# Performance work log

Hardware: AMD Instinct MI355X
Metric: run time of the kernel (lower is better)

The kernel has to match this reference:

```python
import jax, jax.numpy as jnp
import numpy as np

D_MODEL = 768
NUM_HEADS = 12
HEAD_DIM = D_MODEL // NUM_HEADS
D_FF = 3072
LN_EPS = 1e-5


def _xavier(key, shape):
    # nn.init.xavier_uniform_ on a [out, in] Linear weight
    fan_out, fan_in = shape[-2], shape[-1]
    limit = float(np.sqrt(6.0 / (fan_in + fan_out)))
    return jax.random.uniform(key, shape, jnp.float32, -limit, limit)


def setup_inputs() -> dict:
    key = jax.random.key(0)
    ks = jax.random.split(key, 10)
    x = jax.random.normal(ks[0], (4, 2048, D_MODEL), jnp.float32)
    # per-head projections stacked: [H, head_dim, d_model] (torch Linear weight layout [out, in])
    Wq = _xavier(ks[1], (NUM_HEADS, HEAD_DIM, D_MODEL))
    Wk = _xavier(ks[2], (NUM_HEADS, HEAD_DIM, D_MODEL))
    Wv = _xavier(ks[3], (NUM_HEADS, HEAD_DIM, D_MODEL))
    Wo = _xavier(ks[4], (D_MODEL, D_MODEL))
    W1 = jax.random.normal(ks[5], (D_FF, D_MODEL), jnp.float32) * 0.02
    b1 = jnp.zeros((D_FF,), jnp.float32)
    W2 = jax.random.normal(ks[6], (D_MODEL, D_FF), jnp.float32) * 0.02
    b2 = jnp.zeros((D_MODEL,), jnp.float32)
    g1 = jnp.ones((D_MODEL,), jnp.float32)
    be1 = jnp.zeros((D_MODEL,), jnp.float32)
    g2 = jnp.ones((D_MODEL,), jnp.float32)
    be2 = jnp.zeros((D_MODEL,), jnp.float32)
    return {"x": x, "Wq": Wq, "Wk": Wk, "Wv": Wv, "Wo": Wo,
            "W1": W1, "b1": b1, "W2": W2, "b2": b2,
            "g1": g1, "be1": be1, "g2": g2, "be2": be2}


def _layernorm(x, g, b):
    mu = jnp.mean(x, axis=-1, keepdims=True)
    var = jnp.mean(jnp.square(x - mu), axis=-1, keepdims=True)
    return (x - mu) * jax.lax.rsqrt(var + LN_EPS) * g + b


def reference(x, Wq, Wk, Wv, Wo, W1, b1, W2, b2, g1, be1, g2, be2):
    B, S, D = x.shape
    # all heads batched (same math as the per-head Python loop + concat)
    q = jnp.einsum('bsd,hed->bhse', x, Wq)   # [B,H,S,e]
    k = jnp.einsum('bsd,hed->bhse', x, Wk)
    v = jnp.einsum('bsd,hed->bhse', x, Wv)
    scores = jnp.einsum('bhse,bhte->bhst', q, k) / jnp.sqrt(jnp.float32(HEAD_DIM))
    attn = jax.nn.softmax(scores, axis=-1)
    ctx = jnp.einsum('bhst,bhte->bhse', attn, v)
    # concat heads along feature dim (head order matches stacking order)
    concat = ctx.transpose(0, 2, 1, 3).reshape(B, S, D)
    attn_out = concat @ Wo.T
    h = _layernorm(x + attn_out, g1, be1)
    ffn = jax.nn.relu(h @ W1.T + b1) @ W2.T + b2
    out = _layernorm(h + ffn, g2, be2)
    return out
```

## Files before the change

kernel.cpp:

```cpp
#include <hip/hip_runtime.h>

typedef unsigned short u16;
typedef unsigned int u32;
typedef __attribute__((ext_vector_type(8))) short short8;
typedef __attribute__((ext_vector_type(4))) float f32x4;
typedef __attribute__((ext_vector_type(4))) unsigned short u16x4;

__device__ __forceinline__ float b2f(u16 u){
  union { float f; unsigned int i; } c; c.i = ((unsigned int)u) << 16; return c.f;
}
__device__ __forceinline__ u16 f2b(float f){
  union { float f; unsigned int i; } c; c.f = f;
  unsigned int i = c.i;
  unsigned int r = (i + 0x7FFFu + ((i >> 16) & 1u)) >> 16;
  return (u16)r;
}

#define EXP2(x) exp2f(x)

#define GLD16(gp, lp) __builtin_amdgcn_global_load_lds( \
    (const __attribute__((address_space(1))) void*)(gp), \
    (__attribute__((address_space(3))) void*)(lp), 16, 0, 0)

__device__ __forceinline__ u32 pkbf(float lo, float hi){
  u32 r;
  asm volatile("v_cvt_pk_bf16_f32 %0, %1, %2" : "=v"(r) : "v"(lo), "v"(hi));
  return r;
}

__global__ __launch_bounds__(256) void cvt_all(
    const float* __restrict__ s0, const float* __restrict__ s1,
    const float* __restrict__ s2, const float* __restrict__ s3,
    const float* __restrict__ s4, const float* __restrict__ s5,
    const float* __restrict__ s6, u16* __restrict__ dst)
{
  const int i = (blockIdx.x * 256 + threadIdx.x) * 4;
  const float* sp;
  if      (i <  6291456) sp = s0 + i;
  else if (i <  6881280) sp = s1 + (i - 6291456);
  else if (i <  7471104) sp = s2 + (i - 6881280);
  else if (i <  8060928) sp = s3 + (i - 7471104);
  else if (i <  8650752) sp = s4 + (i - 8060928);
  else if (i < 11010048) sp = s5 + (i - 8650752);
  else                   sp = s6 + (i - 11010048);
  float4 f = *(const float4*)sp;
  u16x4 o = { f2b(f.x), f2b(f.y), f2b(f.z), f2b(f.w) };
  *(u16x4*)(dst + i) = o;
}

__global__ __launch_bounds__(256) void transpose_v(const u16* __restrict__ v,
                                                   u16* __restrict__ vt){
  __shared__ short t[64][72];
  const int plane = blockIdx.y;
  const u16* vp = v + (size_t)plane * 2048 * 64;
  u16* vtp = vt + (size_t)plane * 2048 * 64;
  const int s0 = blockIdx.x * 64;
#pragma unroll
  for (int j = 0; j < 2; j++){
    int ch = threadIdx.x + 256*j;
    int r = ch >> 3, c = (ch & 7) << 3;
    short8 val = *(const short8*)(vp + (size_t)(s0 + r)*64 + c);
#pragma unroll
    for (int jj = 0; jj < 8; jj++) t[c + jj][r] = val[jj];
  }
  __syncthreads();
#pragma unroll
  for (int j = 0; j < 2; j++){
    int ch = threadIdx.x + 256*j;
    int r = ch >> 3, c = (ch & 7) << 3;
    *(short8*)(vtp + (size_t)r*2048 + s0 + c) = *(const short8*)&t[r][c];
  }
}

enum { EPI_QKV = 0, EPI_WO = 1, EPI_FFN1 = 2, EPI_FFN2 = 3 };
__device__ __forceinline__ float KSCALE_C(){ return 0.125f * 1.44269504088896340736f; }

template<int EPI>
__global__ __launch_bounds__(256) void gemm_bt(
    const u16* __restrict__ A, const u16* __restrict__ Bm,
    int K, int gx,
    u16* __restrict__ outB,
    const float* __restrict__ auxF,
    const u16* __restrict__ auxB)
{
  __shared__ __align__(16) short Asm[128][32];
  __shared__ __align__(16) short Bsm[128][32];
  const int tid  = threadIdx.x;
  const int lane = tid & 63;
  const int wid  = tid >> 6;
  const int wr = wid >> 1, wc = wid & 1;
  const int fr = lane & 15, fq = lane >> 4;

  const int nwg = gridDim.x;
  const int lin = blockIdx.x;
  const int wg  = (lin & 7) * (nwg >> 3) + (lin >> 3);
  const int bx = wg % gx, by = wg / gx;
  const int m0 = by * 128, n0 = bx * 128;

  f32x4 acc[4][4];
#pragma unroll
  for (int i = 0; i < 4; i++)
#pragma unroll
    for (int j = 0; j < 4; j++) acc[i][j] = (f32x4){0.f, 0.f, 0.f, 0.f};

  const int lrow = lane >> 2;
  const int lcol = (lane & 3) << 3;

  for (int k0 = 0; k0 < K; k0 += 32) {
    const u16* ga = A  + (size_t)(m0 + wid*32 + lrow) * K + k0 + lcol;
    const u16* gb = Bm + (size_t)(n0 + wid*32 + lrow) * K + k0 + lcol;
    GLD16(ga,                 &Asm[wid*32][0]);
    GLD16(ga + (size_t)16*K,  &Asm[wid*32 + 16][0]);
    GLD16(gb,                 &Bsm[wid*32][0]);
    GLD16(gb + (size_t)16*K,  &Bsm[wid*32 + 16][0]);
    __syncthreads();

    short8 a[4], b[4];
#pragma unroll
    for (int i = 0; i < 4; i++) a[i] = *(const short8*)&Asm[wr*64 + i*16 + fr][fq*8];
#pragma unroll
    for (int j = 0; j < 4; j++) b[j] = *(const short8*)&Bsm[wc*64 + j*16 + fr][fq*8];
    __builtin_amdgcn_s_setprio(1);
#pragma unroll
    for (int i = 0; i < 4; i++)
#pragma unroll
      for (int j = 0; j < 4; j++)
        acc[i][j] = __builtin_amdgcn_mfma_f32_16x16x32_bf16(a[i], b[j], acc[i][j], 0, 0, 0);
    __builtin_amdgcn_s_setprio(0);
    __syncthreads();
  }

#pragma unroll
  for (int i = 0; i < 4; i++) {
    const int row0 = m0 + wr*64 + i*16 + fq*4;
#pragma unroll
    for (int j = 0; j < 4; j++) {
      const int col = n0 + wc*64 + j*16 + fr;
#pragma unroll
      for (int r = 0; r < 4; r++) {
        const int row = row0 + r;
        float val = acc[i][j][r];
        if (EPI == EPI_QKV) {
          int tt = (col >= 1536) ? 2 : (col >= 768 ? 1 : 0);
          int rem = col - tt * 768;
          int h = rem >> 6, e = rem & 63;
          int bb = row >> 11, s = row & 2047;
          size_t idx = (((size_t)(tt*48 + bb*12 + h)) * 2048 + s) * 64 + e;
          if (tt == 1) val *= KSCALE_C();
          outB[idx] = f2b(val);
        } else if (EPI == EPI_WO) {
          size_t idx = (size_t)row * 768 + col;
          outB[idx] = f2b(val + b2f(auxB[idx]));
        } else if (EPI == EPI_FFN1) {
          float o = val + auxF[col];
          o = o > 0.f ? o : 0.f;
          outB[(size_t)row * 3072 + col] = f2b(o);
        } else {
          size_t idx = (size_t)row * 768 + col;
          outB[idx] = f2b(val + auxF[col] + b2f(auxB[idx]));
        }
      }
    }
  }
}

__global__ __launch_bounds__(256) void flash_attn(
    const u16* __restrict__ q, const u16* __restrict__ kmat, const u16* __restrict__ vtmat,
    u16* __restrict__ ctx)
{
  const int tid = threadIdx.x;
  const int lane = tid & 63, wid = tid >> 6;
  const int fr = lane & 15, fq = lane >> 4;
  const int orig = blockIdx.x;
  const int wg = (orig & 7) * 192 + (orig >> 3);
  const int qb = wg & 31;
  const int ph = wg >> 5;
  const size_t plane = (size_t)ph * 2048 * 64;
  const u16* qp  = q + plane;
  const u16* kp  = kmat + plane;
  const u16* vtp = vtmat + plane;

  __shared__ __align__(16) short Ksm[2][64][64];
  __shared__ __align__(16) short Vsm[2][64][64];

  const int qr0 = qb*64 + wid*16;
  const short8 aq0 = *(const short8*)(qp + (size_t)(qr0 + fr)*64 + fq*8);
  const short8 aq1 = *(const short8*)(qp + (size_t)(qr0 + fr)*64 + 32 + fq*8);

  short8 vones;
#pragma unroll
  for (int j = 0; j < 8; j++) vones[j] = (short)0x3F80;

  const int rA = wid*16 + (lane >> 3);
  const int rB = rA + 8;
  const int cA = (((lane & 7) ^ ((rA & 3) | (((rA >> 3) & 1) << 2)))) * 8;
  const int cB = (((lane & 7) ^ ((rB & 3) | (((rB >> 3) & 1) << 2)))) * 8;

#define STAGE(B, KT) do { \
    GLD16(kp  + (size_t)((KT)*64 + rA)*64 + cA,  &Ksm[B][wid*16    ][0]); \
    GLD16(kp  + (size_t)((KT)*64 + rB)*64 + cB,  &Ksm[B][wid*16 + 8][0]); \
    GLD16(vtp + (size_t)rA*2048 + (KT)*64 + cA,  &Vsm[B][wid*16    ][0]); \
    GLD16(vtp + (size_t)rB*2048 + (KT)*64 + cB,  &Vsm[B][wid*16 + 8][0]); \
  } while(0)

  f32x4 o[4];
#pragma unroll
  for (int eb = 0; eb < 4; eb++) o[eb] = (f32x4){0.f, 0.f, 0.f, 0.f};
  float m = -1e30f, l = 0.f;
  const f32x4 zero = (f32x4){0.f, 0.f, 0.f, 0.f};

  STAGE(0, 0);
  __syncthreads();

  const int fK  = (fr & 3) | (((fr >> 2) & 1) << 2);
  const int kc0 = ((fq    ) ^ fK) * 8;
  const int kc1 = ((4 + fq) ^ fK) * 8;
  const int krow = (fr & 3) + 8 * (fr >> 2);
  const int fV  = (fr & 3) | (((fr >> 3) & 1) << 2);
  const int vc0 = ((fq    ) ^ fV) * 8;
  const int vc1 = ((4 + fq) ^ fV) * 8;

  int buf = 0;
  for (int kt = 0; kt < 32; ++kt) {
    if (kt < 31) STAGE(buf ^ 1, kt + 1);

    f32x4 st[2][2];
    __builtin_amdgcn_s_setprio(1);
#pragma unroll
    for (int h = 0; h < 2; h++)
#pragma unroll
      for (int c = 0; c < 2; c++) {
        const short* kr = &Ksm[buf][32*h + 4*c + krow][0];
        short8 kf0 = *(const short8*)(kr + kc0);
        short8 kf1 = *(const short8*)(kr + kc1);
        f32x4 a = __builtin_amdgcn_mfma_f32_16x16x32_bf16(kf0, aq0, zero, 0, 0, 0);
        st[h][c]  = __builtin_amdgcn_mfma_f32_16x16x32_bf16(kf1, aq1, a,    0, 0, 0);
      }
    __builtin_amdgcn_s_setprio(0);

    float t0 = fmaxf(fmaxf(st[0][0][0], st[0][0][1]), st[0][0][2]);
    float t1 = fmaxf(fmaxf(st[0][0][3], st[0][1][0]), st[0][1][1]);
    float t2 = fmaxf(fmaxf(st[0][1][2], st[0][1][3]), st[1][0][0]);
    float t3 = fmaxf(fmaxf(st[1][0][1], st[1][0][2]), st[1][0][3]);
    float t4 = fmaxf(fmaxf(st[1][1][0], st[1][1][1]), st[1][1][2]);
    float u0 = fmaxf(fmaxf(t0, t1), st[1][1][3]);
    float u1 = fmaxf(fmaxf(t2, t3), t4);
    float lm = fmaxf(u0, u1);
    lm = fmaxf(lm, __shfl_xor(lm, 16));
    lm = fmaxf(lm, __shfl_xor(lm, 32));

    if (!__all(lm <= m + 8.f)) {
      float nm = fmaxf(m, lm);
      float corr = EXP2(m - nm);
      m = nm;
      l *= corr;
#pragma unroll
      for (int eb = 0; eb < 4; eb++)
#pragma unroll
        for (int r = 0; r < 4; r++) o[eb][r] *= corr;
    }

    float p[2][2][4];
#pragma unroll
    for (int h = 0; h < 2; h++)
#pragma unroll
      for (int c = 0; c < 2; c++)
#pragma unroll
        for (int r = 0; r < 4; r++)
          p[h][c][r] = EXP2(st[h][c][r] - m);

    union { u32 u[4]; short8 s8; } pf0, pf1;
    pf0.u[0] = pkbf(p[0][0][0], p[0][0][1]);
    pf0.u[1] = pkbf(p[0][0][2], p[0][0][3]);
    pf0.u[2] = pkbf(p[0][1][0], p[0][1][1]);
    pf0.u[3] = pkbf(p[0][1][2], p[0][1][3]);
    pf1.u[0] = pkbf(p[1][0][0], p[1][0][1]);
    pf1.u[1] = pkbf(p[1][0][2], p[1][0][3]);
    pf1.u[2] = pkbf(p[1][1][0], p[1][1][1]);
    pf1.u[3] = pkbf(p[1][1][2], p[1][1][3]);

    __builtin_amdgcn_s_setprio(1);
    f32x4 ol = __builtin_amdgcn_mfma_f32_16x16x32_bf16(vones, pf0.s8, zero, 0, 0, 0);
    ol       = __builtin_amdgcn_mfma_f32_16x16x32_bf16(vones, pf1.s8, ol,   0, 0, 0);
#pragma unroll
    for (int eb = 0; eb < 4; eb++) {
      const short* vr = &Vsm[buf][eb*16 + fr][0];
      o[eb] = __builtin_amdgcn_mfma_f32_16x16x32_bf16(*(const short8*)(vr + vc0), pf0.s8, o[eb], 0, 0, 0);
      o[eb] = __builtin_amdgcn_mfma_f32_16x16x32_bf16(*(const short8*)(vr + vc1), pf1.s8, o[eb], 0, 0, 0);
    }
    __builtin_amdgcn_s_setprio(0);
    l += ol[0];

    __syncthreads();
    buf ^= 1;
  }
#undef STAGE

  const float inv = 1.0f / l;
  const int s = qr0 + fr;
  u16* cp = ctx + ((size_t)((ph/12)*2048 + s)) * 768 + (ph%12)*64;
#pragma unroll
  for (int eb = 0; eb < 4; eb++) {
    u16x4 w = { f2b(o[eb][0]*inv), f2b(o[eb][1]*inv), f2b(o[eb][2]*inv), f2b(o[eb][3]*inv) };
    *(u16x4*)(cp + eb*16 + fq*4) = w;
  }
}

template<int F32OUT>
__global__ __launch_bounds__(256) void ln_k(const u16* __restrict__ in,
    const float* __restrict__ g, const float* __restrict__ be, void* __restrict__ outp)
{
  const int lane = threadIdx.x & 63, wid = threadIdx.x >> 6;
  const int row = blockIdx.x * 4 + wid;
  const u16* p = in + (size_t)row * 768;
  float v[12];
  float s = 0.f, s2 = 0.f;
#pragma unroll
  for (int i = 0; i < 6; i++) {
    ushort2 uv = *(const ushort2*)(p + i*128 + lane*2);
    v[2*i]   = b2f(uv.x);
    v[2*i+1] = b2f(uv.y);
    s += v[2*i] + v[2*i+1];
    s2 += v[2*i]*v[2*i] + v[2*i+1]*v[2*i+1];
  }
#pragma unroll
  for (int msk = 1; msk < 64; msk <<= 1) { s += __shfl_xor(s, msk); s2 += __shfl_xor(s2, msk); }
  const float mu = s * (1.f/768.f);
  const float var = s2 * (1.f/768.f) - mu*mu;
  const float rstd = rsqrtf(var + 1e-5f);
#pragma unroll
  for (int i = 0; i < 6; i++) {
    int c = i*128 + lane*2;
    float o0 = (v[2*i]   - mu) * rstd * g[c]   + be[c];
    float o1 = (v[2*i+1] - mu) * rstd * g[c+1] + be[c+1];
    if (F32OUT) {
      float2 w = { o0, o1 };
      *(float2*)((float*)outp + (size_t)row*768 + c) = w;
    } else {
      ushort2 w = { f2b(o0), f2b(o1) };
      *(ushort2*)((u16*)outp + (size_t)row*768 + c) = w;
    }
  }
}

extern "C" void kernel_launch(void* const* d_in, const int* in_sizes, int n_in,
                              void* d_out, int out_size, void* d_ws, size_t ws_size,
                              hipStream_t stream)
{
  const float* x   = (const float*)d_in[0];
  const float* Wq  = (const float*)d_in[1];
  const float* Wk  = (const float*)d_in[2];
  const float* Wv  = (const float*)d_in[3];
  const float* Wo  = (const float*)d_in[4];
  const float* W1  = (const float*)d_in[5];
  const float* b1  = (const float*)d_in[6];
  const float* W2  = (const float*)d_in[7];
  const float* b2  = (const float*)d_in[8];
  const float* g1  = (const float*)d_in[9];
  const float* be1 = (const float*)d_in[10];
  const float* g2  = (const float*)d_in[11];
  const float* be2 = (const float*)d_in[12];
  float* out = (float*)d_out;

  char* ws = (char*)d_ws;
  u16* xb     = (u16*)(ws + 0);
  u16* Wqkv_b = (u16*)(ws + 12582912);
  u16* Wo_b   = (u16*)(ws + 16121856);
  u16* W1_b   = (u16*)(ws + 17301504);
  u16* W2_b   = (u16*)(ws + 22020096);
  u16* qkv    = (u16*)(ws + 26738688);
  u16* ctxb   = (u16*)(ws + 64487424);
  u16* hidden = (u16*)(ws + 26738688);
  u16* vt     = (u16*)(ws + 77070336);
  u16* resid1 = (u16*)(ws + 77070336);
  u16* hb     = (u16*)(ws + 102236160);
  u16* pre2   = (u16*)(ws + 77070336);

  cvt_all<<<dim3(13056), 256, 0, stream>>>(x, Wq, Wk, Wv, Wo, W1, W2, (u16*)ws);

  gemm_bt<EPI_QKV><<<dim3(1152), 256, 0, stream>>>(
      xb, Wqkv_b, 768, 18, qkv, nullptr, nullptr);

  u16* qb_ = qkv;
  u16* kb_ = qkv + 6291456;
  u16* vb_ = qkv + 12582912;

  transpose_v<<<dim3(32, 48), 256, 0, stream>>>(vb_, vt);

  flash_attn<<<dim3(1536), 256, 0, stream>>>(qb_, kb_, vt, ctxb);

  gemm_bt<EPI_WO><<<dim3(384), 256, 0, stream>>>(
      ctxb, Wo_b, 768, 6, resid1, nullptr, xb);

  ln_k<0><<<2048, 256, 0, stream>>>(resid1, g1, be1, hb);

  gemm_bt<EPI_FFN1><<<dim3(1536), 256, 0, stream>>>(
      hb, W1_b, 768, 24, hidden, b1, nullptr);

  gemm_bt<EPI_FFN2><<<dim3(384), 256, 0, stream>>>(
      hidden, W2_b, 3072, 6, pre2, b2, hb);

  ln_k<1><<<2048, 256, 0, stream>>>(pre2, g2, be2, out);
}
```

Measured before the change: 328.3 us.

## Use 64x128 GEMM tiles for QKV/Wo/FFN2 and 128-row flash-attn blocks

Adds a gemm_bt64 kernel with 64x128 output tiles, used for the QKV, Wo and FFN2 projections. This doubles the grid size so the small-N GEMMs fill more compute units. The original 128x128 gemm_bt is kept only for FFN1. Flash attention moves to 512-thread blocks covering 128 query rows, so each staged K/V tile is shared by 8 waves, which halves the number of K/V tile loads. The cost is less reuse per GEMM tile and possibly lower occupancy for the larger attention blocks.

Result: no change. 323.2 us (-1.6%).

```diff
diff --git a/kernel.cpp b/kernel.cpp
--- a/kernel.cpp
+++ b/kernel.cpp
@@ -133,6 +133,80 @@
 #pragma unroll
   for (int i = 0; i < 4; i++) {
     const int row0 = m0 + wr*64 + i*16 + fq*4;
+#pragma unroll
+    for (int j = 0; j < 4; j++) {
+      const int col = n0 + wc*64 + j*16 + fr;
+#pragma unroll
+      for (int r = 0; r < 4; r++) {
+        const int row = row0 + r;
+        float val = acc[i][j][r];
+        if (EPI == EPI_FFN1) {
+          float o = val + auxF[col];
+          o = o > 0.f ? o : 0.f;
+          outB[(size_t)row * 3072 + col] = f2b(o);
+        }
+      }
+    }
+  }
+}
+
+template<int EPI>
+__global__ __launch_bounds__(256) void gemm_bt64(
+    const u16* __restrict__ A, const u16* __restrict__ Bm,
+    int K, int gx,
+    u16* __restrict__ outB,
+    const float* __restrict__ auxF,
+    const u16* __restrict__ auxB)
+{
+  __shared__ __align__(16) short Asm[64][32];
+  __shared__ __align__(16) short Bsm[128][32];
+  const int tid  = threadIdx.x;
+  const int lane = tid & 63;
+  const int wid  = tid >> 6;
+  const int wr = wid >> 1, wc = wid & 1;
+  const int fr = lane & 15, fq = lane >> 4;
+
+  const int nwg = gridDim.x;
+  const int lin = blockIdx.x;
+  const int wg  = (lin & 7) * (nwg >> 3) + (lin >> 3);
+  const int bx = wg % gx, by = wg / gx;
+  const int m0 = by * 64, n0 = bx * 128;
+
+  f32x4 acc[2][4];
+#pragma unroll
+  for (int i = 0; i < 2; i++)
+#pragma unroll
+    for (int j = 0; j < 4; j++) acc[i][j] = (f32x4){0.f, 0.f, 0.f, 0.f};
+
+  const int lrow = lane >> 2;
+  const int lcol = (lane & 3) << 3;
+
+  for (int k0 = 0; k0 < K; k0 += 32) {
+    const u16* ga = A  + (size_t)(m0 + wid*16 + lrow) * K + k0 + lcol;
+    const u16* gb = Bm + (size_t)(n0 + wid*32 + lrow) * K + k0 + lcol;
+    GLD16(ga,                 &Asm[wid*16][0]);
+    GLD16(gb,                 &Bsm[wid*32][0]);
+    GLD16(gb + (size_t)16*K,  &Bsm[wid*32 + 16][0]);
+    __syncthreads();
+
+    short8 a[2], b[4];
+#pragma unroll
+    for (int i = 0; i < 2; i++) a[i] = *(const short8*)&Asm[wr*32 + i*16 + fr][fq*8];
+#pragma unroll
+    for (int j = 0; j < 4; j++) b[j] = *(const short8*)&Bsm[wc*64 + j*16 + fr][fq*8];
+    __builtin_amdgcn_s_setprio(1);
+#pragma unroll
+    for (int i = 0; i < 2; i++)
+#pragma unroll
+      for (int j = 0; j < 4; j++)
+        acc[i][j] = __builtin_amdgcn_mfma_f32_16x16x32_bf16(a[i], b[j], acc[i][j], 0, 0, 0);
+    __builtin_amdgcn_s_setprio(0);
+    __syncthreads();
+  }
+
+#pragma unroll
+  for (int i = 0; i < 2; i++) {
+    const int row0 = m0 + wr*32 + i*16 + fq*4;
 #pragma unroll
     for (int j = 0; j < 4; j++) {
       const int col = n0 + wc*64 + j*16 + fr;
@@ -151,10 +225,6 @@
         } else if (EPI == EPI_WO) {
           size_t idx = (size_t)row * 768 + col;
           outB[idx] = f2b(val + b2f(auxB[idx]));
-        } else if (EPI == EPI_FFN1) {
-          float o = val + auxF[col];
-          o = o > 0.f ? o : 0.f;
-          outB[(size_t)row * 3072 + col] = f2b(o);
         } else {
           size_t idx = (size_t)row * 768 + col;
           outB[idx] = f2b(val + auxF[col] + b2f(auxB[idx]));
@@ -164,7 +234,7 @@
   }
 }
 
-__global__ __launch_bounds__(256) void flash_attn(
+__global__ __launch_bounds__(512) void flash_attn(
     const u16* __restrict__ q, const u16* __restrict__ kmat, const u16* __restrict__ vtmat,
     u16* __restrict__ ctx)
 {
@@ -172,9 +242,9 @@
   const int lane = tid & 63, wid = tid >> 6;
   const int fr = lane & 15, fq = lane >> 4;
   const int orig = blockIdx.x;
-  const int wg = (orig & 7) * 192 + (orig >> 3);
-  const int qb = wg & 31;
-  const int ph = wg >> 5;
+  const int wg = (orig & 7) * 96 + (orig >> 3);
+  const int qb = wg & 15;
+  const int ph = wg >> 4;
   const size_t plane = (size_t)ph * 2048 * 64;
   const u16* qp  = q + plane;
   const u16* kp  = kmat + plane;
@@ -183,7 +253,7 @@
   __shared__ __align__(16) short Ksm[2][64][64];
   __shared__ __align__(16) short Vsm[2][64][64];
 
-  const int qr0 = qb*64 + wid*16;
+  const int qr0 = qb*128 + wid*16;
   const short8 aq0 = *(const short8*)(qp + (size_t)(qr0 + fr)*64 + fq*8);
   const short8 aq1 = *(const short8*)(qp + (size_t)(qr0 + fr)*64 + 32 + fq*8);
 
@@ -191,16 +261,12 @@
 #pragma unroll
   for (int j = 0; j < 8; j++) vones[j] = (short)0x3F80;
 
-  const int rA = wid*16 + (lane >> 3);
-  const int rB = rA + 8;
+  const int rA = wid*8 + (lane >> 3);
   const int cA = (((lane & 7) ^ ((rA & 3) | (((rA >> 3) & 1) << 2)))) * 8;
-  const int cB = (((lane & 7) ^ ((rB & 3) | (((rB >> 3) & 1) << 2)))) * 8;
 
 #define STAGE(B, KT) do { \
-    GLD16(kp  + (size_t)((KT)*64 + rA)*64 + cA,  &Ksm[B][wid*16    ][0]); \
-    GLD16(kp  + (size_t)((KT)*64 + rB)*64 + cB,  &Ksm[B][wid*16 + 8][0]); \
-    GLD16(vtp + (size_t)rA*2048 + (KT)*64 + cA,  &Vsm[B][wid*16    ][0]); \
-    GLD16(vtp + (size_t)rB*2048 + (KT)*64 + cB,  &Vsm[B][wid*16 + 8][0]); \
+    GLD16(kp  + (size_t)((KT)*64 + rA)*64 + cA,  &Ksm[B][wid*8][0]); \
+    GLD16(vtp + (size_t)rA*2048 + (KT)*64 + cA,  &Vsm[B][wid*8][0]); \
   } while(0)
 
   f32x4 o[4];
@@ -378,7 +444,7 @@
 
   cvt_all<<<dim3(13056), 256, 0, stream>>>(x, Wq, Wk, Wv, Wo, W1, W2, (u16*)ws);
 
-  gemm_bt<EPI_QKV><<<dim3(1152), 256, 0, stream>>>(
+  gemm_bt64<EPI_QKV><<<dim3(2304), 256, 0, stream>>>(
       xb, Wqkv_b, 768, 18, qkv, nullptr, nullptr);
 
   u16* qb_ = qkv;
@@ -387,9 +453,9 @@
 
   transpose_v<<<dim3(32, 48), 256, 0, stream>>>(vb_, vt);
 
-  flash_attn<<<dim3(1536), 256, 0, stream>>>(qb_, kb_, vt, ctxb);
-
-  gemm_bt<EPI_WO><<<dim3(384), 256, 0, stream>>>(
+  flash_attn<<<dim3(768), 512, 0, stream>>>(qb_, kb_, vt, ctxb);
+
+  gemm_bt64<EPI_WO><<<dim3(768), 256, 0, stream>>>(
       ctxb, Wo_b, 768, 6, resid1, nullptr, xb);
 
   ln_k<0><<<2048, 256, 0, stream>>>(resid1, g1, be1, hb);
@@ -397,7 +463,7 @@
   gemm_bt<EPI_FFN1><<<dim3(1536), 256, 0, stream>>>(
       hb, W1_b, 768, 24, hidden, b1, nullptr);
 
-  gemm_bt<EPI_FFN2><<<dim3(384), 256, 0, stream>>>(
+  gemm_bt64<EPI_FFN2><<<dim3(768), 256, 0, stream>>>(
       hidden, W2_b, 3072, 6, pre2, b2, hb);
 
   ln_k<1><<<2048, 256, 0, stream>>>(pre2, g2, be2, out);
```

## Use 512-thread flash-attention blocks and fold running max into MFMA accumulator init

Applied to the files above, without the earlier changes.

Each attention workgroup now has 8 waves covering 128 query rows, so each staged 64-key K/V tile serves twice as many rows and each thread issues half as many global-to-LDS loads. The running maximum is kept as a negated offset and fed in as the initial accumulator of the QK^T MFMA, which removes the per-element subtraction before exp2 in the common no-rescale path. The trade-off is half as many blocks (768), with a larger block that may lower occupancy and scheduling flexibility. The epilogue outside the shown hunks must still match the new row mapping.

Measured after the change: 321.2 us. 1.02x faster.

```diff
diff --git a/kernel.cpp b/kernel.cpp
--- a/kernel.cpp
+++ b/kernel.cpp
@@ -164,7 +164,7 @@
   }
 }
 
-__global__ __launch_bounds__(256) void flash_attn(
+__global__ __launch_bounds__(512) void flash_attn(
     const u16* __restrict__ q, const u16* __restrict__ kmat, const u16* __restrict__ vtmat,
     u16* __restrict__ ctx)
 {
@@ -172,9 +172,9 @@
   const int lane = tid & 63, wid = tid >> 6;
   const int fr = lane & 15, fq = lane >> 4;
   const int orig = blockIdx.x;
-  const int wg = (orig & 7) * 192 + (orig >> 3);
-  const int qb = wg & 31;
-  const int ph = wg >> 5;
+  const int wg = (orig & 7) * 96 + (orig >> 3);
+  const int qb = wg & 15;
+  const int ph = wg >> 4;
   const size_t plane = (size_t)ph * 2048 * 64;
   const u16* qp  = q + plane;
   const u16* kp  = kmat + plane;
@@ -183,7 +183,7 @@
   __shared__ __align__(16) short Ksm[2][64][64];
   __shared__ __align__(16) short Vsm[2][64][64];
 
-  const int qr0 = qb*64 + wid*16;
+  const int qr0 = qb*128 + wid*16;
   const short8 aq0 = *(const short8*)(qp + (size_t)(qr0 + fr)*64 + fq*8);
   const short8 aq1 = *(const short8*)(qp + (size_t)(qr0 + fr)*64 + 32 + fq*8);
 
@@ -191,22 +191,18 @@
 #pragma unroll
   for (int j = 0; j < 8; j++) vones[j] = (short)0x3F80;
 
-  const int rA = wid*16 + (lane >> 3);
-  const int rB = rA + 8;
+  const int rA = wid*8 + (lane >> 3);
   const int cA = (((lane & 7) ^ ((rA & 3) | (((rA >> 3) & 1) << 2)))) * 8;
-  const int cB = (((lane & 7) ^ ((rB & 3) | (((rB >> 3) & 1) << 2)))) * 8;
 
 #define STAGE(B, KT) do { \
-    GLD16(kp  + (size_t)((KT)*64 + rA)*64 + cA,  &Ksm[B][wid*16    ][0]); \
-    GLD16(kp  + (size_t)((KT)*64 + rB)*64 + cB,  &Ksm[B][wid*16 + 8][0]); \
-    GLD16(vtp + (size_t)rA*2048 + (KT)*64 + cA,  &Vsm[B][wid*16    ][0]); \
-    GLD16(vtp + (size_t)rB*2048 + (KT)*64 + cB,  &Vsm[B][wid*16 + 8][0]); \
+    GLD16(kp  + (size_t)((KT)*64 + rA)*64 + cA,  &Ksm[B][wid*8][0]); \
+    GLD16(vtp + (size_t)rA*2048 + (KT)*64 + cA,  &Vsm[B][wid*8][0]); \
   } while(0)
 
   f32x4 o[4];
 #pragma unroll
   for (int eb = 0; eb < 4; eb++) o[eb] = (f32x4){0.f, 0.f, 0.f, 0.f};
-  float m = -1e30f, l = 0.f;
+  float mneg = 0.f, l = 0.f;
   const f32x4 zero = (f32x4){0.f, 0.f, 0.f, 0.f};
 
   STAGE(0, 0);
@@ -225,6 +221,7 @@
     if (kt < 31) STAGE(buf ^ 1, kt + 1);
 
     f32x4 st[2][2];
+    const f32x4 cini = (f32x4){mneg, mneg, mneg, mneg};
     __builtin_amdgcn_s_setprio(1);
 #pragma unroll
     for (int h = 0; h < 2; h++)
@@ -233,7 +230,7 @@
         const short* kr = &Ksm[buf][32*h + 4*c + krow][0];
         short8 kf0 = *(const short8*)(kr + kc0);
         short8 kf1 = *(const short8*)(kr + kc1);
-        f32x4 a = __builtin_amdgcn_mfma_f32_16x16x32_bf16(kf0, aq0, zero, 0, 0, 0);
+        f32x4 a = __builtin_amdgcn_mfma_f32_16x16x32_bf16(kf0, aq0, cini, 0, 0, 0);
         st[h][c]  = __builtin_amdgcn_mfma_f32_16x16x32_bf16(kf1, aq1, a,    0, 0, 0);
       }
     __builtin_amdgcn_s_setprio(0);
@@ -249,25 +246,32 @@
     lm = fmaxf(lm, __shfl_xor(lm, 16));
     lm = fmaxf(lm, __shfl_xor(lm, 32));
 
-    if (!__all(lm <= m + 8.f)) {
-      float nm = fmaxf(m, lm);
-      float corr = EXP2(m - nm);
-      m = nm;
+    float p[2][2][4];
+    if (!__all(lm <= 8.f)) {
+      float d = fmaxf(lm, 0.f);
+      float corr = EXP2(-d);
+      mneg -= d;
       l *= corr;
 #pragma unroll
       for (int eb = 0; eb < 4; eb++)
 #pragma unroll
         for (int r = 0; r < 4; r++) o[eb][r] *= corr;
+#pragma unroll
+      for (int h = 0; h < 2; h++)
+#pragma unroll
+        for (int c = 0; c < 2; c++)
+#pragma unroll
+          for (int r = 0; r < 4; r++)
+            p[h][c][r] = EXP2(st[h][c][r] - d);
+    } else {
+#pragma unroll
+      for (int h = 0; h < 2; h++)
+#pragma unroll
+        for (int c = 0; c < 2; c++)
+#pragma unroll
+          for (int r = 0; r < 4; r++)
+            p[h][c][r] = EXP2(st[h][c][r]);
     }
-
-    float p[2][2][4];
-#pragma unroll
-    for (int h = 0; h < 2; h++)
-#pragma unroll
-      for (int c = 0; c < 2; c++)
-#pragma unroll
-        for (int r = 0; r < 4; r++)
-          p[h][c][r] = EXP2(st[h][c][r] - m);
 
     union { u32 u[4]; short8 s8; } pf0, pf1;
     pf0.u[0] = pkbf(p[0][0][0], p[0][0][1]);
@@ -387,7 +391,7 @@
 
   transpose_v<<<dim3(32, 48), 256, 0, stream>>>(vb_, vt);
 
-  flash_attn<<<dim3(1536), 256, 0, stream>>>(qb_, kb_, vt, ctxb);
+  flash_attn<<<dim3(768), 512, 0, stream>>>(qb_, kb_, vt, ctxb);
 
   gemm_bt<EPI_WO><<<dim3(384), 256, 0, stream>>>(
       ctxb, Wo_b, 768, 6, resid1, nullptr, xb);
```
